# Performance work log

Hardware: AMD Instinct MI355X
Metric: run time of the kernel (lower is better)

## Reference

```python
import jax, jax.numpy as jnp
import numpy as np

B, S, D, H = 2, 2048, 1024, 16
DK = D // H


def setup_inputs() -> dict:
    key = jax.random.key(0)
    ks = jax.random.split(key, 12)
    std = 1.0 / np.sqrt(D)
    inp = {
        "query": jax.random.normal(ks[0], (B, S, D), jnp.float32),
        "key": jax.random.normal(ks[1], (B, S, D), jnp.float32),
        "value": jax.random.normal(ks[2], (B, S, D), jnp.float32),
        # causal mask: 1 = keep, 0 = blocked (matches masked_fill(mask==0, -inf))
        "mask": jnp.tril(jnp.ones((S, S), jnp.int32))[None, None, :, :],
        # torch Linear convention: W is (out, in), y = x @ W.T + b
        "Wq": jax.random.normal(ks[3], (D, D), jnp.float32) * std,
        "bq": jax.random.normal(ks[4], (D,), jnp.float32) * std,
        "Wk": jax.random.normal(ks[5], (D, D), jnp.float32) * std,
        "bk": jax.random.normal(ks[6], (D,), jnp.float32) * std,
        "Wv": jax.random.normal(ks[7], (D, D), jnp.float32) * std,
        "bv": jax.random.normal(ks[8], (D,), jnp.float32) * std,
        "Wo": jax.random.normal(ks[9], (D, D), jnp.float32) * std,
        "bo": jax.random.normal(ks[10], (D,), jnp.float32) * std,
    }
    return inp


def reference(query, key, value, mask, Wq, bq, Wk, bk, Wv, bv, Wo, bo):
    b = query.shape[0]
    # projections (torch Linear: x @ W.T + b)
    Q = query @ Wq.T + bq
    K = key @ Wk.T + bk
    V = value @ Wv.T + bv
    # (b, s, d) -> (b, h, s, dk)
    Q = Q.reshape(b, -1, H, DK).transpose(0, 2, 1, 3)
    K = K.reshape(b, -1, H, DK).transpose(0, 2, 1, 3)
    V = V.reshape(b, -1, H, DK).transpose(0, 2, 1, 3)
    scores = jnp.einsum("bhqd,bhkd->bhqk", Q, K) / jnp.sqrt(jnp.float32(DK))
    scores = jnp.where(mask == 0, -jnp.inf, scores)
    weights = jax.nn.softmax(scores, axis=-1)  # dropout p=0.0 / eval mode: no-op
    attn = jnp.einsum("bhqk,bhkd->bhqd", weights, V)
    attn = attn.transpose(0, 2, 1, 3).reshape(b, -1, D)
    return attn @ Wo.T + bo
```

## Files before the change

### kernel.cpp

```cpp
#include <hip/hip_runtime.h>
#include <hip/hip_bf16.h>
#include <cstdint>
#include <cstddef>


#define B_ 2
#define S_ 2048
#define D_ 1024
#define H_ 16
#define DK_ 64
#define QSCALE 0.1803368801111244f

typedef __attribute__((ext_vector_type(8))) short bf16x8;
typedef __attribute__((ext_vector_type(4))) float f32x4;
typedef __attribute__((ext_vector_type(16))) float f32x16;
typedef __attribute__((ext_vector_type(4))) unsigned short u16x4;
typedef __attribute__((ext_vector_type(4))) float float4v;
typedef __attribute__((ext_vector_type(2))) unsigned int u32x2;
typedef __attribute__((ext_vector_type(4))) unsigned int u32x4;

__device__ __forceinline__ unsigned short f2bf(float f) {
  unsigned int u = __float_as_uint(f);
  u += 0x7FFFu + ((u >> 16) & 1u);
  return (unsigned short)(u >> 16);
}
__device__ __forceinline__ unsigned int cvt_pk_bf16(float lo, float hi) {
  unsigned int r;
  asm("v_cvt_pk_bf16_f32 %0, %1, %2" : "=v"(r) : "v"(lo), "v"(hi));
  return r;
}

__global__ __launch_bounds__(256) void cvt3(const float* __restrict__ s0,
                                            const float* __restrict__ s1,
                                            const float* __restrict__ s2,
                                            unsigned short* __restrict__ d0,
                                            unsigned short* __restrict__ d1,
                                            unsigned short* __restrict__ d2) {
  const float* src = blockIdx.y == 0 ? s0 : blockIdx.y == 1 ? s1 : s2;
  unsigned short* dst = blockIdx.y == 0 ? d0 : blockIdx.y == 1 ? d1 : d2;
  int i = blockIdx.x * 256 + threadIdx.x;
  float4v v = *(const float4v*)(src + (size_t)i * 4);
  u16x4 o;
  o[0] = f2bf(v[0]); o[1] = f2bf(v[1]); o[2] = f2bf(v[2]); o[3] = f2bf(v[3]);
  *(u16x4*)(dst + (size_t)i * 4) = o;
}

__global__ __launch_bounds__(256) void cvt4(const float* __restrict__ s0,
                                            const float* __restrict__ s1,
                                            const float* __restrict__ s2,
                                            const float* __restrict__ s3,
                                            unsigned short* __restrict__ d0,
                                            unsigned short* __restrict__ d1,
                                            unsigned short* __restrict__ d2,
                                            unsigned short* __restrict__ d3) {
  int z = blockIdx.y;
  const float* src = z == 0 ? s0 : z == 1 ? s1 : z == 2 ? s2 : s3;
  unsigned short* dst = z == 0 ? d0 : z == 1 ? d1 : z == 2 ? d2 : d3;
  int i = blockIdx.x * 256 + threadIdx.x;
  float4v v = *(const float4v*)(src + (size_t)i * 4);
  u16x4 o;
  o[0] = f2bf(v[0]); o[1] = f2bf(v[1]); o[2] = f2bf(v[2]); o[3] = f2bf(v[3]);
  *(u16x4*)(dst + (size_t)i * 4) = o;
}

__global__ __launch_bounds__(256) void gemm_qkv(
    const unsigned short* __restrict__ Xq, const unsigned short* __restrict__ Xk,
    const unsigned short* __restrict__ Xv, const unsigned short* __restrict__ Wq,
    const unsigned short* __restrict__ Wk, const unsigned short* __restrict__ Wv,
    const float* __restrict__ bq, const float* __restrict__ bk,
    const float* __restrict__ bv, unsigned short* __restrict__ Qp,
    unsigned short* __restrict__ Kp, unsigned short* __restrict__ Vt) {
  const int z = blockIdx.z;
  const unsigned short* A = z == 0 ? Xq : z == 1 ? Xk : Xv;
  const unsigned short* W = z == 0 ? Wq : z == 1 ? Wk : Wv;
  const float* bias = z == 0 ? bq : z == 1 ? bk : bv;
  const int K = D_, N = D_;

  __shared__ __align__(16) unsigned short As[128 * 64];
  __shared__ __align__(16) unsigned short Bs[128 * 64];
  const int tid  = threadIdx.x;
  const int lane = tid & 63;
  const int m0 = blockIdx.x * 128;
  const int n0 = blockIdx.y * 128;
  const int wr = ((tid >> 6) >> 1) * 64;
  const int wc = ((tid >> 6) & 1) * 64;
  const int lr = lane & 15;
  const int lk = (lane >> 4) * 8;
  f32x4 acc[4][4] = {};

  const int chunkrow = tid >> 3;
  const int chunkcol = (tid & 7) * 8;

  for (int k0 = 0; k0 < K; k0 += 64) {
    __syncthreads();
#pragma unroll
    for (int i = 0; i < 4; ++i) {
      int row = chunkrow + i * 32;
      const unsigned short* gA = A + (size_t)(m0 + row) * K + k0 + chunkcol;
      const unsigned short* gB = W + (size_t)(n0 + row) * K + k0 + chunkcol;
      __builtin_amdgcn_global_load_lds((const __attribute__((address_space(1))) void*)gA,
          (__attribute__((address_space(3))) void*)(As + row * 64 + chunkcol), 16, 0, 0);
      __builtin_amdgcn_global_load_lds((const __attribute__((address_space(1))) void*)gB,
          (__attribute__((address_space(3))) void*)(Bs + row * 64 + chunkcol), 16, 0, 0);
    }
    __syncthreads();
#pragma unroll
    for (int kk = 0; kk < 2; ++kk) {
      bf16x8 a[4], b[4];
#pragma unroll
      for (int m = 0; m < 4; ++m)
        a[m] = *(const bf16x8*)(As + (wr + m * 16 + lr) * 64 + kk * 32 + lk);
#pragma unroll
      for (int n = 0; n < 4; ++n)
        b[n] = *(const bf16x8*)(Bs + (wc + n * 16 + lr) * 64 + kk * 32 + lk);
#pragma unroll
      for (int m = 0; m < 4; ++m)
#pragma unroll
        for (int n = 0; n < 4; ++n)
          acc[m][n] = __builtin_amdgcn_mfma_f32_16x16x32_bf16(a[m], b[n], acc[m][n], 0, 0, 0);
    }
  }

  const int rbase = (lane >> 4) * 4;
  if (z == 2) {
#pragma unroll
    for (int m = 0; m < 4; ++m)
#pragma unroll
      for (int n = 0; n < 4; ++n) {
        int col = n0 + wc + n * 16 + lr;
        float bvv = bias[col];
        int row0 = m0 + wr + m * 16 + rbase;
        int bb = row0 >> 11, s = row0 & 2047;
        int h = col >> 6, dk = col & 63;
        u16x4 o;
#pragma unroll
        for (int r = 0; r < 4; ++r) o[r] = f2bf(acc[m][n][r] + bvv);
        size_t idx = (((size_t)bb * H_ + h) * DK_ + dk) * S_ + s;
        *(u16x4*)(Vt + idx) = o;
      }
  } else {
    unsigned short* Cout = z == 0 ? Qp : Kp;
    const float scale = z == 0 ? QSCALE : 1.0f;
#pragma unroll
    for (int m = 0; m < 4; ++m)
#pragma unroll
      for (int n = 0; n < 4; ++n) {
        int col = n0 + wc + n * 16 + lr;
        float bvv = bias[col];
#pragma unroll
        for (int r = 0; r < 4; ++r) {
          int row = m0 + wr + m * 16 + rbase + r;
          Cout[(size_t)row * N + col] = f2bf((acc[m][n][r] + bvv) * scale);
        }
      }
  }
}

__global__ __launch_bounds__(256) void gemm_o(const unsigned short* __restrict__ A,
                                              const unsigned short* __restrict__ W,
                                              const float* __restrict__ bias,
                                              float* __restrict__ C,
                                              int M, int N, int K) {
  __shared__ __align__(16) unsigned short As[64 * 64];
  __shared__ __align__(16) unsigned short Bs[128 * 64];
  const int tid  = threadIdx.x;
  const int lane = tid & 63;
  const int m0 = blockIdx.x * 64;
  const int n0 = blockIdx.y * 128;
  const int wr = ((tid >> 6) >> 1) * 32;
  const int wc = ((tid >> 6) & 1) * 64;
  const int lr = lane & 15;
  const int lk = (lane >> 4) * 8;
  f32x4 acc[2][4] = {};

  const int chunkrow = tid >> 3;
  const int chunkcol = (tid & 7) * 8;

  for (int k0 = 0; k0 < K; k0 += 64) {
    __syncthreads();
#pragma unroll
    for (int i = 0; i < 2; ++i) {
      int row = chunkrow + i * 32;
      const unsigned short* gA = A + (size_t)(m0 + row) * K + k0 + chunkcol;
      __builtin_amdgcn_global_load_lds((const __attribute__((address_space(1))) void*)gA,
          (__attribute__((address_space(3))) void*)(As + row * 64 + chunkcol), 16, 0, 0);
    }
#pragma unroll
    for (int i = 0; i < 4; ++i) {
      int row = chunkrow + i * 32;
      const unsigned short* gB = W + (size_t)(n0 + row) * K + k0 + chunkcol;
      __builtin_amdgcn_global_load_lds((const __attribute__((address_space(1))) void*)gB,
          (__attribute__((address_space(3))) void*)(Bs + row * 64 + chunkcol), 16, 0, 0);
    }
    __syncthreads();
#pragma unroll
    for (int kk = 0; kk < 2; ++kk) {
      bf16x8 a[2], b[4];
#pragma unroll
      for (int m = 0; m < 2; ++m)
        a[m] = *(const bf16x8*)(As + (wr + m * 16 + lr) * 64 + kk * 32 + lk);
#pragma unroll
      for (int n = 0; n < 4; ++n)
        b[n] = *(const bf16x8*)(Bs + (wc + n * 16 + lr) * 64 + kk * 32 + lk);
#pragma unroll
      for (int m = 0; m < 2; ++m)
#pragma unroll
        for (int n = 0; n < 4; ++n)
          acc[m][n] = __builtin_amdgcn_mfma_f32_16x16x32_bf16(a[m], b[n], acc[m][n], 0, 0, 0);
    }
  }

  const int rbase = (lane >> 4) * 4;
#pragma unroll
  for (int m = 0; m < 2; ++m)
#pragma unroll
    for (int n = 0; n < 4; ++n) {
      int col = n0 + wc + n * 16 + lr;
      float bvv = bias[col];
#pragma unroll
      for (int r = 0; r < 4; ++r) {
        int row = m0 + wr + m * 16 + rbase + r;
        C[(size_t)row * N + col] = acc[m][n][r] + bvv;
      }
    }
}

__device__ __forceinline__ bf16x8 lds_read_swK(const unsigned short* base, int row, int col) {
  int P = (row * 64 + col) * 2;
  int X = P ^ ((row & 7) << 4);
  return *(const bf16x8*)((const char*)base + X);
}
__device__ __forceinline__ bf16x8 lds_read_swV(const unsigned short* base, int row, int col) {
  int P = (row * 128 + col) * 2;
  int X = P ^ ((row & 7) << 4);
  return *(const bf16x8*)((const char*)base + X);
}

__global__ __launch_bounds__(256) void flash_attn(const unsigned short* __restrict__ Qp,
                                                  const unsigned short* __restrict__ Kp,
                                                  const unsigned short* __restrict__ Vtp,
                                                  unsigned short* __restrict__ Op) {
  __shared__ __align__(16) unsigned short smem[128 * 64 + 64 * 128];
  unsigned short* Kb = smem;
  unsigned short* Vb = smem + 128 * 64;

  const int tid  = threadIdx.x;
  const int lane = tid & 63;
  const int w = tid >> 6;
  const int qh = w & 1;
  const int kp = w >> 1;
  const int h  = blockIdx.y;
  const int b  = blockIdx.z;
  const int qt = (blockIdx.x + 4 * (h & 7) + 8 * (h >> 3) + 16 * b) & 31;
  const int q0 = qt * 64;
  const int ql = lane & 31;
  const int hi5 = lane >> 5;
  const int qbase = q0 + qh * 32;
  const int qglob = qbase + ql;
  const size_t basebs = (size_t)b * S_ * D_;
  const int hoff = h * DK_;

  bf16x8 qf[4];
  {
    const unsigned short* qrow = Qp + basebs + (size_t)qglob * D_ + hoff;
#pragma unroll
    for (int f = 0; f < 4; ++f)
      qf[f] = *(const bf16x8*)(qrow + f * 16 + hi5 * 8);
  }

  float m_r = -1e30f;
  float l_r = 0.f;
  f32x16 out0 = {};
  f32x16 out1 = {};

  const unsigned short* gK0 = Kp + basebs + hoff;
  const unsigned short* gV0 = Vtp + ((size_t)b * H_ + h) * DK_ * S_;

  int dstXK[4], srcK[4], dstXV[4], srcV[4];
#pragma unroll
  for (int i = 0; i < 4; ++i) {
    int X = tid * 16 + i * 4096;
    int Pk = X ^ (((X >> 7) & 7) << 4);
    dstXK[i] = X;
    srcK[i] = (Pk >> 7) * D_ + ((Pk & 127) >> 1);
    int Pv = X ^ (((X >> 8) & 7) << 4);
    dstXV[i] = X;
    srcV[i] = (Pv >> 8) * S_ + ((Pv & 255) >> 1);
  }

  const int R = (qt + 2) >> 1;

  for (int r = 0; r < R; ++r) {
    __syncthreads();
    {
      const unsigned short* gK = gK0 + (size_t)(r * 128) * D_;
      const unsigned short* gV = gV0 + r * 128;
#pragma unroll
      for (int i = 0; i < 4; ++i) {
        __builtin_amdgcn_global_load_lds(
            (const __attribute__((address_space(1))) void*)(gK + srcK[i]),
            (__attribute__((address_space(3))) void*)((char*)Kb + dstXK[i]), 16, 0, 0);
        __builtin_amdgcn_global_load_lds(
            (const __attribute__((address_space(1))) void*)(gV + srcV[i]),
            (__attribute__((address_space(3))) void*)((char*)Vb + dstXV[i]), 16, 0, 0);
      }
    }
    __syncthreads();

    const int kv0w = r * 128 + kp * 64;
    const bool do0 = (kv0w <= qbase);
    const bool do1 = (kv0w + 32 <= qbase);
    const bool part0 = (kv0w == qbase);
    const bool part1 = (kv0w + 32 == qbase);
    if (!do0) continue;

    f32x16 sc0 = {}, sc1 = {};
    __builtin_amdgcn_s_setprio(1);
#pragma unroll
    for (int f = 0; f < 4; ++f) {
      bf16x8 kf = lds_read_swK(Kb, kp * 64 + ql, f * 16 + hi5 * 8);
      sc0 = __builtin_amdgcn_mfma_f32_32x32x16_bf16(kf, qf[f], sc0, 0, 0, 0);
    }
    if (do1) {
#pragma unroll
      for (int f = 0; f < 4; ++f) {
        bf16x8 kf = lds_read_swK(Kb, kp * 64 + 32 + ql, f * 16 + hi5 * 8);
        sc1 = __builtin_amdgcn_mfma_f32_32x32x16_bf16(kf, qf[f], sc1, 0, 0, 0);
      }
    }
    __builtin_amdgcn_s_setprio(0);

    if (part0) {
#pragma unroll
      for (int g = 0; g < 16; ++g) {
        int kvg = kv0w + (g & 3) + 8 * (g >> 2) + 4 * hi5;
        if (kvg > qglob) sc0[g] = -1e30f;
      }
    }
    if (do1 && part1) {
#pragma unroll
      for (int g = 0; g < 16; ++g) {
        int kvg = kv0w + 32 + (g & 3) + 8 * (g >> 2) + 4 * hi5;
        if (kvg > qglob) sc1[g] = -1e30f;
      }
    }

    float pm = sc0[0];
#pragma unroll
    for (int g = 1; g < 16; ++g) pm = fmaxf(pm, sc0[g]);
    if (do1) {
#pragma unroll
      for (int g = 0; g < 16; ++g) pm = fmaxf(pm, sc1[g]);
    }
    pm = fmaxf(pm, __shfl_xor(pm, 32));

    if (!__all(pm - m_r <= 8.0f)) {
      float mnew = fmaxf(m_r, pm);
      float scl = __builtin_exp2f(m_r - mnew);
      l_r *= scl;
#pragma unroll
      for (int g = 0; g < 16; ++g) { out0[g] *= scl; out1[g] *= scl; }
      m_r = mnew;
    }

    float l_add = 0.f;
#define PV_CHUNK(SVEC, HALF, C)                                                \
    {                                                                          \
      const int g0 = (HALF) * 8;                                               \
      float p0 = __builtin_exp2f((SVEC)[g0 + 0] - m_r);                        \
      float p1 = __builtin_exp2f((SVEC)[g0 + 1] - m_r);                        \
      float p2 = __builtin_exp2f((SVEC)[g0 + 2] - m_r);                        \
      float p3 = __builtin_exp2f((SVEC)[g0 + 3] - m_r);                        \
      float p4 = __builtin_exp2f((SVEC)[g0 + 4] - m_r);                        \
      float p5 = __builtin_exp2f((SVEC)[g0 + 5] - m_r);                        \
      float p6 = __builtin_exp2f((SVEC)[g0 + 6] - m_r);                        \
      float p7 = __builtin_exp2f((SVEC)[g0 + 7] - m_r);                        \
      l_add += ((p0 + p1) + (p2 + p3)) + ((p4 + p5) + (p6 + p7));              \
      unsigned int u0 = cvt_pk_bf16(p0, p1);                                   \
      unsigned int u1 = cvt_pk_bf16(p2, p3);                                   \
      unsigned int u2 = cvt_pk_bf16(p4, p5);                                   \
      unsigned int u3 = cvt_pk_bf16(p6, p7);                                   \
      unsigned int ta = hi5 ? u0 : u2, tb = hi5 ? u1 : u3;                     \
      unsigned int ra = (unsigned int)__shfl_xor((int)ta, 32);                 \
      unsigned int rb = (unsigned int)__shfl_xor((int)tb, 32);                 \
      u32x4 pw = {hi5 ? ra : u0, hi5 ? rb : u1, hi5 ? u2 : ra, hi5 ? u3 : rb}; \
      bf16x8 pf = __builtin_bit_cast(bf16x8, pw);                              \
      bf16x8 vf0 = lds_read_swV(Vb, ql, kp * 64 + (C) * 16 + hi5 * 8);         \
      out0 = __builtin_amdgcn_mfma_f32_32x32x16_bf16(vf0, pf, out0, 0, 0, 0);  \
      bf16x8 vf1 = lds_read_swV(Vb, 32 + ql, kp * 64 + (C) * 16 + hi5 * 8);    \
      out1 = __builtin_amdgcn_mfma_f32_32x32x16_bf16(vf1, pf, out1, 0, 0, 0);  \
    }
    __builtin_amdgcn_s_setprio(1);
    PV_CHUNK(sc0, 0, 0);
    PV_CHUNK(sc0, 1, 1);
    if (do1) {
      PV_CHUNK(sc1, 0, 2);
      PV_CHUNK(sc1, 1, 3);
    }
    __builtin_amdgcn_s_setprio(0);
#undef PV_CHUNK

    l_add += __shfl_xor(l_add, 32);
    l_r += l_add;
  }

  __syncthreads();
  float* scr = (float*)smem;
  if (kp == 1) {
    float* p = scr + ((size_t)qh * 64 + lane) * 34;
#pragma unroll
    for (int g = 0; g < 16; ++g) { p[g] = out0[g]; p[16 + g] = out1[g]; }
    p[32] = m_r;
    p[33] = l_r;
  }
  __syncthreads();
  if (kp == 0) {
    const float* p = scr + ((size_t)qh * 64 + lane) * 34;
    float m1 = p[32], l1 = p[33];
    float mM = fmaxf(m_r, m1);
    float s0 = __builtin_exp2f(m_r - mM);
    float s1 = __builtin_exp2f(m1 - mM);
    float rcp = 1.0f / (l_r * s0 + l1 * s1);
    float a0 = s0 * rcp, a1 = s1 * rcp;
    unsigned short* orow = Op + basebs + (size_t)qglob * D_ + hoff;
#pragma unroll
    for (int i = 0; i < 4; ++i) {
      u32x2 o0 = {cvt_pk_bf16(out0[4 * i + 0] * a0 + p[4 * i + 0] * a1,
                              out0[4 * i + 1] * a0 + p[4 * i + 1] * a1),
                  cvt_pk_bf16(out0[4 * i + 2] * a0 + p[4 * i + 2] * a1,
                              out0[4 * i + 3] * a0 + p[4 * i + 3] * a1)};
      *(u32x2*)(orow + 8 * i + 4 * hi5) = o0;
      u32x2 o1 = {cvt_pk_bf16(out1[4 * i + 0] * a0 + p[16 + 4 * i + 0] * a1,
                              out1[4 * i + 1] * a0 + p[16 + 4 * i + 1] * a1),
                  cvt_pk_bf16(out1[4 * i + 2] * a0 + p[16 + 4 * i + 2] * a1,
                              out1[4 * i + 3] * a0 + p[16 + 4 * i + 3] * a1)};
      *(u32x2*)(orow + 32 + 8 * i + 4 * hi5) = o1;
    }
  }
}

extern "C" void kernel_launch(void* const* d_in, const int* in_sizes, int n_in,
                              void* d_out, int out_size, void* d_ws, size_t ws_size,
                              hipStream_t stream) {
  const float* q  = (const float*)d_in[0];
  const float* k  = (const float*)d_in[1];
  const float* v  = (const float*)d_in[2];
  const float* Wq = (const float*)d_in[4];
  const float* bq = (const float*)d_in[5];
  const float* Wk = (const float*)d_in[6];
  const float* bk = (const float*)d_in[7];
  const float* Wv = (const float*)d_in[8];
  const float* bv = (const float*)d_in[9];
  const float* Wo = (const float*)d_in[10];
  const float* bo = (const float*)d_in[11];

  const int MSD = B_ * S_;
  unsigned short* ws = (unsigned short*)d_ws;
  unsigned short* Xq  = ws;
  unsigned short* Xk  = Xq  + (size_t)MSD * D_;
  unsigned short* Xv  = Xk  + (size_t)MSD * D_;
  unsigned short* Wqb = Xv  + (size_t)MSD * D_;
  unsigned short* Wkb = Wqb + (size_t)D_ * D_;
  unsigned short* Wvb = Wkb + (size_t)D_ * D_;
  unsigned short* Wob = Wvb + (size_t)D_ * D_;
  unsigned short* Qp  = Wob + (size_t)D_ * D_;
  unsigned short* Kp  = Qp  + (size_t)MSD * D_;
  unsigned short* Vt  = Kp  + (size_t)MSD * D_;
  unsigned short* At  = Vt  + (size_t)MSD * D_;

  const int n4a = MSD * D_ / 4;
  const int n4w = D_ * D_ / 4;
  dim3 g3(n4a / 256, 3);
  cvt3<<<g3, 256, 0, stream>>>(q, k, v, Xq, Xk, Xv);
  dim3 g4(n4w / 256, 4);
  cvt4<<<g4, 256, 0, stream>>>(Wq, Wk, Wv, Wo, Wqb, Wkb, Wvb, Wob);

  dim3 gqkv(MSD / 128, D_ / 128, 3);
  gemm_qkv<<<gqkv, 256, 0, stream>>>(Xq, Xk, Xv, Wqb, Wkb, Wvb,
                                     bq, bk, bv, Qp, Kp, Vt);

  dim3 ga(S_ / 64, H_, B_);
  flash_attn<<<ga, 256, 0, stream>>>(Qp, Kp, Vt, At);

  dim3 go(MSD / 64, D_ / 128);
  gemm_o<<<go, 256, 0, stream>>>(At, Wob, bo, (float*)d_out, MSD, D_, D_);
}
```

Baseline: 161.1 us.

## Double-buffer K/V tiles and pair causal query tiles per attention block

The flash attention kernel now gives each block two query tiles (31-x and x), so every block does the same amount of causal work, and the grid shrinks to 16 blocks along the sequence axis. K/V tiles are double-buffered in 64KB of LDS, and the next tile's global-to-LDS load is issued before computing on the current one, which removes one barrier per iteration. The larger LDS footprint may lower occupancy, and the smaller grid (512 blocks) relies on the balanced per-block work.

```diff
diff --git a/kernel.cpp b/kernel.cpp
--- a/kernel.cpp
+++ b/kernel.cpp
@@ -240,9 +240,7 @@
                                                   const unsigned short* __restrict__ Kp,
                                                   const unsigned short* __restrict__ Vtp,
                                                   unsigned short* __restrict__ Op) {
-  __shared__ __align__(16) unsigned short smem[128 * 64 + 64 * 128];
-  unsigned short* Kb = smem;
-  unsigned short* Vb = smem + 128 * 64;
+  __shared__ __align__(16) unsigned short smem[32768];
 
   const int tid  = threadIdx.x;
   const int lane = tid & 63;
@@ -251,32 +249,15 @@
   const int kp = w >> 1;
   const int h  = blockIdx.y;
   const int b  = blockIdx.z;
-  const int qt = (blockIdx.x + 4 * (h & 7) + 8 * (h >> 3) + 16 * b) & 31;
-  const int q0 = qt * 64;
   const int ql = lane & 31;
   const int hi5 = lane >> 5;
-  const int qbase = q0 + qh * 32;
-  const int qglob = qbase + ql;
   const size_t basebs = (size_t)b * S_ * D_;
   const int hoff = h * DK_;
 
-  bf16x8 qf[4];
-  {
-    const unsigned short* qrow = Qp + basebs + (size_t)qglob * D_ + hoff;
-#pragma unroll
-    for (int f = 0; f < 4; ++f)
-      qf[f] = *(const bf16x8*)(qrow + f * 16 + hi5 * 8);
-  }
-
-  float m_r = -1e30f;
-  float l_r = 0.f;
-  f32x16 out0 = {};
-  f32x16 out1 = {};
-
   const unsigned short* gK0 = Kp + basebs + hoff;
   const unsigned short* gV0 = Vtp + ((size_t)b * H_ + h) * DK_ * S_;
 
-  int dstXK[4], srcK[4], dstXV[4], srcV[4];
+  int dstXK[4], srcK[4], srcV[4];
 #pragma unroll
   for (int i = 0; i < 4; ++i) {
     int X = tid * 16 + i * 4096;
@@ -284,159 +265,192 @@
     dstXK[i] = X;
     srcK[i] = (Pk >> 7) * D_ + ((Pk & 127) >> 1);
     int Pv = X ^ (((X >> 8) & 7) << 4);
-    dstXV[i] = X;
     srcV[i] = (Pv >> 8) * S_ + ((Pv & 255) >> 1);
   }
 
-  const int R = (qt + 2) >> 1;
-
-  for (int r = 0; r < R; ++r) {
-    __syncthreads();
+#define STAGE(RR, BUF)                                                         \
+  {                                                                            \
+    const unsigned short* gK = gK0 + (size_t)((RR) * 128) * D_;                \
+    const unsigned short* gV = gV0 + (RR) * 128;                               \
+    char* kb = (char*)smem + (BUF) * 32768;                                    \
+    char* vb = kb + 16384;                                                     \
+    _Pragma("unroll")                                                          \
+    for (int i = 0; i < 4; ++i) {                                              \
+      __builtin_amdgcn_global_load_lds(                                        \
+          (const __attribute__((address_space(1))) void*)(gK + srcK[i]),       \
+          (__attribute__((address_space(3))) void*)(kb + dstXK[i]), 16, 0, 0); \
+      __builtin_amdgcn_global_load_lds(                                        \
+          (const __attribute__((address_space(1))) void*)(gV + srcV[i]),       \
+          (__attribute__((address_space(3))) void*)(vb + dstXK[i]), 16, 0, 0); \
+    }                                                                          \
+  }
+
+  for (int s = 0; s < 2; ++s) {
+    const int qt = s == 0 ? 31 - (int)blockIdx.x : (int)blockIdx.x;
+    const int q0 = qt * 64;
+    const int qbase = q0 + qh * 32;
+    const int qglob = qbase + ql;
+
+    bf16x8 qf[4];
     {
-      const unsigned short* gK = gK0 + (size_t)(r * 128) * D_;
-      const unsigned short* gV = gV0 + r * 128;
+      const unsigned short* qrow = Qp + basebs + (size_t)qglob * D_ + hoff;
+#pragma unroll
+      for (int f = 0; f < 4; ++f)
+        qf[f] = *(const bf16x8*)(qrow + f * 16 + hi5 * 8);
+    }
+
+    float m_r = -1e30f;
+    float l_r = 0.f;
+    f32x16 out0 = {};
+    f32x16 out1 = {};
+
+    const int R = (qt + 2) >> 1;
+
+    STAGE(0, 0);
+    __syncthreads();
+
+    for (int r = 0; r < R; ++r) {
+      const int cur = r & 1;
+      if (r + 1 < R) STAGE(r + 1, cur ^ 1);
+
+      const unsigned short* Kb = smem + cur * 16384;
+      const unsigned short* Vb = Kb + 8192;
+
+      const int kv0w = r * 128 + kp * 64;
+      const bool do0 = (kv0w <= qbase);
+      const bool do1 = (kv0w + 32 <= qbase);
+      const bool part0 = (kv0w == qbase);
+      const bool part1 = (kv0w + 32 == qbase);
+
+      if (do0) {
+        f32x16 sc0 = {}, sc1 = {};
+        __builtin_amdgcn_s_setprio(1);
+#pragma unroll
+        for (int f = 0; f < 4; ++f) {
+          bf16x8 kf = lds_read_swK(Kb, kp * 64 + ql, f * 16 + hi5 * 8);
+          sc0 = __builtin_amdgcn_mfma_f32_32x32x16_bf16(kf, qf[f], sc0, 0, 0, 0);
+        }
+        if (do1) {
+#pragma unroll
+          for (int f = 0; f < 4; ++f) {
+            bf16x8 kf = lds_read_swK(Kb, kp * 64 + 32 + ql, f * 16 + hi5 * 8);
+            sc1 = __builtin_amdgcn_mfma_f32_32x32x16_bf16(kf, qf[f], sc1, 0, 0, 0);
+          }
+        }
+        __builtin_amdgcn_s_setprio(0);
+
+        if (part0) {
+#pragma unroll
+          for (int g = 0; g < 16; ++g) {
+            int kvg = kv0w + (g & 3) + 8 * (g >> 2) + 4 * hi5;
+            if (kvg > qglob) sc0[g] = -1e30f;
+          }
+        }
+        if (do1 && part1) {
+#pragma unroll
+          for (int g = 0; g < 16; ++g) {
+            int kvg = kv0w + 32 + (g & 3) + 8 * (g >> 2) + 4 * hi5;
+            if (kvg > qglob) sc1[g] = -1e30f;
+          }
+        }
+
+        float pm = sc0[0];
+#pragma unroll
+        for (int g = 1; g < 16; ++g) pm = fmaxf(pm, sc0[g]);
+        if (do1) {
+#pragma unroll
+          for (int g = 0; g < 16; ++g) pm = fmaxf(pm, sc1[g]);
+        }
+        pm = fmaxf(pm, __shfl_xor(pm, 32));
+
+        if (!__all(pm - m_r <= 8.0f)) {
+          float mnew = fmaxf(m_r, pm);
+          float scl = __builtin_exp2f(m_r - mnew);
+          l_r *= scl;
+#pragma unroll
+          for (int g = 0; g < 16; ++g) { out0[g] *= scl; out1[g] *= scl; }
+          m_r = mnew;
+        }
+
+        float l_add = 0.f;
+#define PV_CHUNK(SVEC, HALF, C)                                                \
+        {                                                                      \
+          const int g0 = (HALF) * 8;                                           \
+          float p0 = __builtin_exp2f((SVEC)[g0 + 0] - m_r);                    \
+          float p1 = __builtin_exp2f((SVEC)[g0 + 1] - m_r);                    \
+          float p2 = __builtin_exp2f((SVEC)[g0 + 2] - m_r);                    \
+          float p3 = __builtin_exp2f((SVEC)[g0 + 3] - m_r);                    \
+          float p4 = __builtin_exp2f((SVEC)[g0 + 4] - m_r);                    \
+          float p5 = __builtin_exp2f((SVEC)[g0 + 5] - m_r);                    \
+          float p6 = __builtin_exp2f((SVEC)[g0 + 6] - m_r);                    \
+          float p7 = __builtin_exp2f((SVEC)[g0 + 7] - m_r);                    \
+          l_add += ((p0 + p1) + (p2 + p3)) + ((p4 + p5) + (p6 + p7));          \
+          unsigned int u0 = cvt_pk_bf16(p0, p1);                               \
+          unsigned int u1 = cvt_pk_bf16(p2, p3);                               \
+          unsigned int u2 = cvt_pk_bf16(p4, p5);                               \
+          unsigned int u3 = cvt_pk_bf16(p6, p7);                               \
+          unsigned int ta = hi5 ? u0 : u2, tb = hi5 ? u1 : u3;                 \
+          unsigned int ra = (unsigned int)__shfl_xor((int)ta, 32);             \
+          unsigned int rb = (unsigned int)__shfl_xor((int)tb, 32);             \
+          u32x4 pw = {hi5 ? ra : u0, hi5 ? rb : u1,                            \
+                      hi5 ? u2 : ra, hi5 ? u3 : rb};                           \
+          bf16x8 pf = __builtin_bit_cast(bf16x8, pw);                          \
+          bf16x8 vf0 = lds_read_swV(Vb, ql, kp * 64 + (C) * 16 + hi5 * 8);     \
+          out0 = __builtin_amdgcn_mfma_f32_32x32x16_bf16(vf0, pf, out0, 0, 0, 0);\
+          bf16x8 vf1 = lds_read_swV(Vb, 32 + ql, kp * 64 + (C) * 16 + hi5 * 8);\
+          out1 = __builtin_amdgcn_mfma_f32_32x32x16_bf16(vf1, pf, out1, 0, 0, 0);\
+        }
+        __builtin_amdgcn_s_setprio(1);
+        PV_CHUNK(sc0, 0, 0);
+        PV_CHUNK(sc0, 1, 1);
+        if (do1) {
+          PV_CHUNK(sc1, 0, 2);
+          PV_CHUNK(sc1, 1, 3);
+        }
+        __builtin_amdgcn_s_setprio(0);
+#undef PV_CHUNK
+
+        l_add += __shfl_xor(l_add, 32);
+        l_r += l_add;
+      }
+      __syncthreads();
+    }
+
+    float* scr = (float*)smem;
+    if (kp == 1) {
+      float* p = scr + ((size_t)qh * 64 + lane) * 34;
+#pragma unroll
+      for (int g = 0; g < 16; ++g) { p[g] = out0[g]; p[16 + g] = out1[g]; }
+      p[32] = m_r;
+      p[33] = l_r;
+    }
+    __syncthreads();
+    if (kp == 0) {
+      const float* p = scr + ((size_t)qh * 64 + lane) * 34;
+      float m1 = p[32], l1 = p[33];
+      float mM = fmaxf(m_r, m1);
+      float s0 = __builtin_exp2f(m_r - mM);
+      float s1 = __builtin_exp2f(m1 - mM);
+      float rcp = 1.0f / (l_r * s0 + l1 * s1);
+      float a0 = s0 * rcp, a1 = s1 * rcp;
+      unsigned short* orow = Op + basebs + (size_t)qglob * D_ + hoff;
 #pragma unroll
       for (int i = 0; i < 4; ++i) {
-        __builtin_amdgcn_global_load_lds(
-            (const __attribute__((address_space(1))) void*)(gK + srcK[i]),
-            (__attribute__((address_space(3))) void*)((char*)Kb + dstXK[i]), 16, 0, 0);
-        __builtin_amdgcn_global_load_lds(
-            (const __attribute__((address_space(1))) void*)(gV + srcV[i]),
-            (__attribute__((address_space(3))) void*)((char*)Vb + dstXV[i]), 16, 0, 0);
+        u32x2 o0 = {cvt_pk_bf16(out0[4 * i + 0] * a0 + p[4 * i + 0] * a1,
+                                out0[4 * i + 1] * a0 + p[4 * i + 1] * a1),
+                    cvt_pk_bf16(out0[4 * i + 2] * a0 + p[4 * i + 2] * a1,
+                                out0[4 * i + 3] * a0 + p[4 * i + 3] * a1)};
+        *(u32x2*)(orow + 8 * i + 4 * hi5) = o0;
+        u32x2 o1 = {cvt_pk_bf16(out1[4 * i + 0] * a0 + p[16 + 4 * i + 0] * a1,
+                                out1[4 * i + 1] * a0 + p[16 + 4 * i + 1] * a1),
+                    cvt_pk_bf16(out1[4 * i + 2] * a0 + p[16 + 4 * i + 2] * a1,
+                                out1[4 * i + 3] * a0 + p[16 + 4 * i + 3] * a1)};
+        *(u32x2*)(orow + 32 + 8 * i + 4 * hi5) = o1;
       }
     }
     __syncthreads();
-
-    const int kv0w = r * 128 + kp * 64;
-    const bool do0 = (kv0w <= qbase);
-    const bool do1 = (kv0w + 32 <= qbase);
-    const bool part0 = (kv0w == qbase);
-    const bool part1 = (kv0w + 32 == qbase);
-    if (!do0) continue;
-
-    f32x16 sc0 = {}, sc1 = {};
-    __builtin_amdgcn_s_setprio(1);
-#pragma unroll
-    for (int f = 0; f < 4; ++f) {
-      bf16x8 kf = lds_read_swK(Kb, kp * 64 + ql, f * 16 + hi5 * 8);
-      sc0 = __builtin_amdgcn_mfma_f32_32x32x16_bf16(kf, qf[f], sc0, 0, 0, 0);
-    }
-    if (do1) {
-#pragma unroll
-      for (int f = 0; f < 4; ++f) {
-        bf16x8 kf = lds_read_swK(Kb, kp * 64 + 32 + ql, f * 16 + hi5 * 8);
-        sc1 = __builtin_amdgcn_mfma_f32_32x32x16_bf16(kf, qf[f], sc1, 0, 0, 0);
-      }
-    }
-    __builtin_amdgcn_s_setprio(0);
-
-    if (part0) {
-#pragma unroll
-      for (int g = 0; g < 16; ++g) {
-        int kvg = kv0w + (g & 3) + 8 * (g >> 2) + 4 * hi5;
-        if (kvg > qglob) sc0[g] = -1e30f;
-      }
-    }
-    if (do1 && part1) {
-#pragma unroll
-      for (int g = 0; g < 16; ++g) {
-        int kvg = kv0w + 32 + (g & 3) + 8 * (g >> 2) + 4 * hi5;
-        if (kvg > qglob) sc1[g] = -1e30f;
-      }
-    }
-
-    float pm = sc0[0];
-#pragma unroll
-    for (int g = 1; g < 16; ++g) pm = fmaxf(pm, sc0[g]);
-    if (do1) {
-#pragma unroll
-      for (int g = 0; g < 16; ++g) pm = fmaxf(pm, sc1[g]);
-    }
-    pm = fmaxf(pm, __shfl_xor(pm, 32));
-
-    if (!__all(pm - m_r <= 8.0f)) {
-      float mnew = fmaxf(m_r, pm);
-      float scl = __builtin_exp2f(m_r - mnew);
-      l_r *= scl;
-#pragma unroll
-      for (int g = 0; g < 16; ++g) { out0[g] *= scl; out1[g] *= scl; }
-      m_r = mnew;
-    }
-
-    float l_add = 0.f;
-#define PV_CHUNK(SVEC, HALF, C)                                                \
-    {                                                                          \
-      const int g0 = (HALF) * 8;                                               \
-      float p0 = __builtin_exp2f((SVEC)[g0 + 0] - m_r);                        \
-      float p1 = __builtin_exp2f((SVEC)[g0 + 1] - m_r);                        \
-      float p2 = __builtin_exp2f((SVEC)[g0 + 2] - m_r);                        \
-      float p3 = __builtin_exp2f((SVEC)[g0 + 3] - m_r);                        \
-      float p4 = __builtin_exp2f((SVEC)[g0 + 4] - m_r);                        \
-      float p5 = __builtin_exp2f((SVEC)[g0 + 5] - m_r);                        \
-      float p6 = __builtin_exp2f((SVEC)[g0 + 6] - m_r);                        \
-      float p7 = __builtin_exp2f((SVEC)[g0 + 7] - m_r);                        \
-      l_add += ((p0 + p1) + (p2 + p3)) + ((p4 + p5) + (p6 + p7));              \
-      unsigned int u0 = cvt_pk_bf16(p0, p1);                                   \
-      unsigned int u1 = cvt_pk_bf16(p2, p3);                                   \
-      unsigned int u2 = cvt_pk_bf16(p4, p5);                                   \
-      unsigned int u3 = cvt_pk_bf16(p6, p7);                                   \
-      unsigned int ta = hi5 ? u0 : u2, tb = hi5 ? u1 : u3;                     \
-      unsigned int ra = (unsigned int)__shfl_xor((int)ta, 32);                 \
-      unsigned int rb = (unsigned int)__shfl_xor((int)tb, 32);                 \
-      u32x4 pw = {hi5 ? ra : u0, hi5 ? rb : u1, hi5 ? u2 : ra, hi5 ? u3 : rb}; \
-      bf16x8 pf = __builtin_bit_cast(bf16x8, pw);                              \
-      bf16x8 vf0 = lds_read_swV(Vb, ql, kp * 64 + (C) * 16 + hi5 * 8);         \
-      out0 = __builtin_amdgcn_mfma_f32_32x32x16_bf16(vf0, pf, out0, 0, 0, 0);  \
-      bf16x8 vf1 = lds_read_swV(Vb, 32 + ql, kp * 64 + (C) * 16 + hi5 * 8);    \
-      out1 = __builtin_amdgcn_mfma_f32_32x32x16_bf16(vf1, pf, out1, 0, 0, 0);  \
-    }
-    __builtin_amdgcn_s_setprio(1);
-    PV_CHUNK(sc0, 0, 0);
-    PV_CHUNK(sc0, 1, 1);
-    if (do1) {
-      PV_CHUNK(sc1, 0, 2);
-      PV_CHUNK(sc1, 1, 3);
-    }
-    __builtin_amdgcn_s_setprio(0);
-#undef PV_CHUNK
-
-    l_add += __shfl_xor(l_add, 32);
-    l_r += l_add;
   }
-
-  __syncthreads();
-  float* scr = (float*)smem;
-  if (kp == 1) {
-    float* p = scr + ((size_t)qh * 64 + lane) * 34;
-#pragma unroll
-    for (int g = 0; g < 16; ++g) { p[g] = out0[g]; p[16 + g] = out1[g]; }
-    p[32] = m_r;
-    p[33] = l_r;
-  }
-  __syncthreads();
-  if (kp == 0) {
-    const float* p = scr + ((size_t)qh * 64 + lane) * 34;
-    float m1 = p[32], l1 = p[33];
-    float mM = fmaxf(m_r, m1);
-    float s0 = __builtin_exp2f(m_r - mM);
-    float s1 = __builtin_exp2f(m1 - mM);
-    float rcp = 1.0f / (l_r * s0 + l1 * s1);
-    float a0 = s0 * rcp, a1 = s1 * rcp;
-    unsigned short* orow = Op + basebs + (size_t)qglob * D_ + hoff;
-#pragma unroll
-    for (int i = 0; i < 4; ++i) {
-      u32x2 o0 = {cvt_pk_bf16(out0[4 * i + 0] * a0 + p[4 * i + 0] * a1,
-                              out0[4 * i + 1] * a0 + p[4 * i + 1] * a1),
-                  cvt_pk_bf16(out0[4 * i + 2] * a0 + p[4 * i + 2] * a1,
-                              out0[4 * i + 3] * a0 + p[4 * i + 3] * a1)};
-      *(u32x2*)(orow + 8 * i + 4 * hi5) = o0;
-      u32x2 o1 = {cvt_pk_bf16(out1[4 * i + 0] * a0 + p[16 + 4 * i + 0] * a1,
-                              out1[4 * i + 1] * a0 + p[16 + 4 * i + 1] * a1),
-                  cvt_pk_bf16(out1[4 * i + 2] * a0 + p[16 + 4 * i + 2] * a1,
-                              out1[4 * i + 3] * a0 + p[16 + 4 * i + 3] * a1)};
-      *(u32x2*)(orow + 32 + 8 * i + 4 * hi5) = o1;
-    }
-  }
+#undef STAGE
 }
 
 extern "C" void kernel_launch(void* const* d_in, const int* in_sizes, int n_in,
@@ -479,7 +493,7 @@
   gemm_qkv<<<gqkv, 256, 0, stream>>>(Xq, Xk, Xv, Wqb, Wkb, Wvb,
                                      bq, bk, bv, Qp, Kp, Vt);
 
-  dim3 ga(S_ / 64, H_, B_);
+  dim3 ga(16, H_, B_);
   flash_attn<<<ga, 256, 0, stream>>>(Qp, Kp, Vt, At);
 
   dim3 go(MSD / 64, D_ / 128);
```

Result: faster. 138.5 us (-14.0%).
